# Performance work log

Measured on AMD Instinct MI355X. Metric: run time of the kernel, lower is better.

Reference implementation:

```python
import jax, jax.numpy as jnp
import numpy as np

B, L, H, D = 4096, 256, 32, 2
LOG_PROB_FACTOR = 0.5

def setup_inputs() -> dict:
    key = jax.random.key(0)
    k0, k1, k2, k3 = jax.random.split(key, 4)
    x = jax.random.randint(k0, (B, L), 0, D)  # spin configs in {0,1}
    Wi = jax.random.normal(k1, (D, 4 * H), dtype=jnp.float32) * 0.1   # input kernel (no bias, flax LSTMCell)
    Wh = jax.random.normal(k2, (H, 4 * H), dtype=jnp.float32) * 0.1   # recurrent kernel
    bh = jnp.zeros((4 * H,), dtype=jnp.float32)                        # recurrent bias
    Wo = jax.random.normal(k3, (H, D), dtype=jnp.float32) * 0.1       # output Dense kernel
    bo = jnp.zeros((D,), dtype=jnp.float32)                            # output Dense bias
    return {"x": x, "Wi": Wi, "Wh": Wh, "bh": bh, "Wo": Wo, "bo": bo}

def reference(x, Wi, Wh, bh, Wo, bo):
    # one-hot of spin t-1 (zeros at t=0); log-prob is read out at spin t.
    x_oh = jax.nn.one_hot(x, D, dtype=Wi.dtype)      # [B, L, D]
    xs = jnp.swapaxes(x_oh, 0, 1)                    # [L, B, D] time-major for scan
    c0 = jnp.zeros((x.shape[0], H), Wi.dtype)
    h0 = jnp.zeros((x.shape[0], H), Wi.dtype)
    inp0 = jnp.zeros((x.shape[0], D), Wi.dtype)      # jnp.zeros(inputDim) initial input

    def step(carry, xt):
        c, h, inp = carry
        gates = inp @ Wi + h @ Wh + bh               # [B, 4H]
        i, f, g, o = jnp.split(gates, 4, axis=-1)    # flax LSTMCell gate order i,f,g,o
        c_new = jax.nn.sigmoid(f) * c + jax.nn.sigmoid(i) * jnp.tanh(g)
        h_new = jax.nn.sigmoid(o) * jnp.tanh(c_new)
        out = jax.nn.elu(h_new @ Wo + bo)            # Dense + actFun, [B, D]
        # log(sum(softmax(out) * onehot)) == gathered log_softmax (stable form)
        logp = jnp.sum(jax.nn.log_softmax(out, axis=-1) * xt, axis=-1)  # [B]
        return (c_new, h_new, xt), logp

    _, logps = jax.lax.scan(step, (c0, h0, inp0), xs)  # logps: [L, B]
    return LOG_PROB_FACTOR * jnp.sum(logps, axis=0)    # [B]
```

## Files before the change

### kernel.cpp

```cpp
#include <hip/hip_runtime.h>


typedef __attribute__((ext_vector_type(8))) short bf16x8;
typedef __attribute__((ext_vector_type(4))) float f32x4;

#define LOG2E 1.4426950408889634f
#define LN2   0.6931471805599453f

__device__ __forceinline__ float fexp2(float x) { return __builtin_amdgcn_exp2f(x); }
__device__ __forceinline__ float flog2(float x) { return __builtin_amdgcn_logf(x); }
__device__ __forceinline__ float frcp(float x)  { return __builtin_amdgcn_rcpf(x); }

__device__ __forceinline__ float fsig(float x)   { return frcp(1.f + fexp2(-LOG2E * x)); }
__device__ __forceinline__ float ftanh_(float x) { return 1.f - 2.f * frcp(fexp2(2.f * LOG2E * x) + 1.f); }
__device__ __forceinline__ float felu(float x)   { return x > 0.f ? x : fexp2(LOG2E * x) - 1.f; }

__device__ __forceinline__ unsigned short f2bf(float f) {
    unsigned u = __builtin_bit_cast(unsigned, f);
    u = (u + 0x7FFFu + ((u >> 16) & 1u)) >> 16;
    return (unsigned short)u;
}

constexpr int Bsz = 4096;

__global__ __launch_bounds__(512, 2) void lstm_r10(
    const int*   __restrict__ x,
    const float* __restrict__ Wi,
    const float* __restrict__ Wh,
    const float* __restrict__ bh,
    const float* __restrict__ Wo,
    const float* __restrict__ bo,
    float*       __restrict__ out)
{
    const int tid  = threadIdx.x;
    const int w    = tid >> 6;
    const int lane = tid & 63;
    const int m    = lane & 15;
    const int oct  = lane >> 4;
    const int rot  = w & 3;
    const int half = w >> 2;
    const int b0   = blockIdx.x * 16;

    __shared__ char   spinT[16][260];
    __shared__ float2 Sbuf[256][16];
    __shared__ short  hbuf[2][16][40];
    __shared__ float  red[8][16];

    {
        const int bl = tid >> 5;
        const int c8 = (tid & 31) * 8;
        const int4* src = reinterpret_cast<const int4*>(x + (b0 + bl) * 256 + c8);
        const int4 v0 = src[0], v1 = src[1];
        const int p0 = (v0.x & 1) | ((v0.y & 1) << 8) | ((v0.z & 1) << 16) | ((v0.w & 1) << 24);
        const int p1 = (v1.x & 1) | ((v1.y & 1) << 8) | ((v1.z & 1) << 16) | ((v1.w & 1) << 24);
        *reinterpret_cast<int*>(&spinT[bl][c8])     = p0;
        *reinterpret_cast<int*>(&spinT[bl][c8 + 4]) = p1;
    }

    bf16x8 wfrag[4];
#pragma unroll
    for (int q = 0; q < 4; ++q) {
        const float gs = (q == 2) ? 2.f * LOG2E : -LOG2E;
        const int colg = 32 * q + 16 * half + ((m + rot) & 15);
#pragma unroll
        for (int j = 0; j < 8; ++j)
            wfrag[q][j] = (short)f2bf(gs * Wh[(oct * 8 + j) * 128 + colg]);
    }
    bf16x8 wofragA;
#pragma unroll
    for (int j = 0; j < 8; ++j)
        wofragA[j] = (m < 2) ? (short)f2bf(Wo[(oct * 8 + j) * 2 + m]) : (short)0;

    const int ucell = 4 * oct + rot + 16 * half;
    float bv0[4], bvd[4];
#pragma unroll
    for (int q = 0; q < 4; ++q) {
        const float gs = (q == 2) ? 2.f * LOG2E : -LOG2E;
        const int c0 = 32 * q + ucell;
        bv0[q] = gs * (bh[c0] + Wi[c0]);
        bvd[q] = gs * (Wi[128 + c0] - Wi[c0]);
    }
    const float bo0 = bo[0], bo1 = bo[1];

    float c = fsig(bh[ucell]) * ftanh_(bh[64 + ucell]);
    hbuf[0][m][ucell] = (short)f2bf(fsig(bh[96 + ucell]) * ftanh_(c));
    __syncthreads();

    const f32x4 zero4 = { 0.f, 0.f, 0.f, 0.f };
    f32x4 ccq[4] = { zero4, zero4, zero4, zero4 };

    auto step = [&](const int t, const int rb, const int wb, const float spf) {
        const bf16x8 hfrag =
            *reinterpret_cast<const bf16x8*>(&hbuf[rb][m][8 * oct]);

#pragma unroll
        for (int q = 0; q < 4; ++q) ccq[q][0] = fmaf(spf, bvd[q], bv0[q]);

        f32x4 acc[4];
#pragma unroll
        for (int q = 0; q < 4; ++q)
            acc[q] = __builtin_amdgcn_mfma_f32_16x16x32_bf16(wfrag[q], hfrag, ccq[q], 0, 0, 0);

        if (((t - 1) & 7) == w) {
            const f32x4 hacc =
                __builtin_amdgcn_mfma_f32_16x16x32_bf16(wofragA, hfrag, zero4, 0, 0, 0);
            if (oct == 0) Sbuf[t - 1][m] = make_float2(hacc[0], hacc[1]);
        }

        {
            const float ei = fexp2(acc[0][0]), ef = fexp2(acc[1][0]);
            const float eg = fexp2(acc[2][0]), eo = fexp2(acc[3][0]);
            const float P = (1.f + ei) * (1.f + eg);
            const float Q = 1.f + ef;
            const float R = frcp(P * Q);
            const float gf  = P * R;
            const float igt = (eg - 1.f) * Q * R;
            c = fmaf(gf, c, igt);
            const float ec = fexp2(2.f * LOG2E * c);
            const float h  = (ec - 1.f) * frcp((1.f + eo) * (1.f + ec));
            hbuf[wb][m][ucell] = (short)f2bf(h);
        }
        __syncthreads();
    };

    unsigned sp2 = *reinterpret_cast<const unsigned short*>(&spinT[m][0]);
    for (int tb = 1; tb < 255; tb += 2) {
        const unsigned sp2n =
            *reinterpret_cast<const unsigned short*>(&spinT[m][tb + 1]);
        step(tb,     0, 1, (float)(sp2 & 0xFFu));
        step(tb + 1, 1, 0, (float)(sp2 >> 8));
        sp2 = sp2n;
    }
    step(255, 0, 1, (float)(sp2 & 0xFFu));

    if (w == 7) {
        const bf16x8 hfrag = *reinterpret_cast<const bf16x8*>(&hbuf[1][m][8 * oct]);
        const f32x4 hacc =
            __builtin_amdgcn_mfma_f32_16x16x32_bf16(wofragA, hfrag, zero4, 0, 0, 0);
        if (oct == 0) Sbuf[255][m] = make_float2(hacc[0], hacc[1]);
    }
    __syncthreads();

    float lp = 0.f;
    {
        const int t0 = (w * 4 + oct) * 8;
#pragma unroll
        for (int i = 0; i < 8; ++i) {
            const int t = t0 + i;
            const float2 sv = Sbuf[t][m];
            const int sp = spinT[m][t];
            const float o0 = felu(sv.x + bo0);
            const float o1 = felu(sv.y + bo1);
            const float mx = fmaxf(o0, o1), mn = fminf(o0, o1);
            const float lse = mx + LN2 * flog2(1.f + fexp2(LOG2E * (mn - mx)));
            lp += (sp ? o1 : o0) - lse;
        }
    }
    lp += __shfl_xor(lp, 16, 64);
    lp += __shfl_xor(lp, 32, 64);
    if (lane < 16) red[w][lane] = lp;
    __syncthreads();
    if (tid < 16) {
        float s = 0.f;
#pragma unroll
        for (int ww = 0; ww < 8; ++ww) s += red[ww][tid];
        out[b0 + tid] = 0.5f * s;
    }
}

extern "C" void kernel_launch(void* const* d_in, const int* in_sizes, int n_in,
                              void* d_out, int out_size, void* d_ws, size_t ws_size,
                              hipStream_t stream) {
    const int*   x  = (const int*)d_in[0];
    const float* Wi = (const float*)d_in[1];
    const float* Wh = (const float*)d_in[2];
    const float* bh = (const float*)d_in[3];
    const float* Wo = (const float*)d_in[4];
    const float* bo = (const float*)d_in[5];
    float* out = (float*)d_out;

    lstm_r10<<<dim3(Bsz / 16), dim3(512), 0, stream>>>(x, Wi, Wh, bh, Wo, bo, out);
}
```

Baseline: 136.2 us.

## Shrink LSTM blocks to 4 batch rows with 2 waves and LDS occupancy padding

Each block now handles 4 batch rows with 2 wavefronts instead of 16 rows with 8 wavefronts, giving four times as many blocks. Each wave covers 16 hidden units across all four gates and picks its row's gate value from the MFMA output lanes. The bias is now added after the MFMA instead of being fed in as the accumulator. A dummy 24 KB shared array caps how many blocks fit per CU, so the blocks spread across CUs. The goal is cheaper per-step barriers (2 waves instead of 8) and more independent recurrences per CU, at the cost of 16-wide MFMA tiles that are only a quarter used on the batch dimension.

Result: slower. 157.2 us (+15.4%).

```diff
diff --git a/kernel.cpp b/kernel.cpp
--- a/kernel.cpp
+++ b/kernel.cpp
@@ -23,7 +23,7 @@
 
 constexpr int Bsz = 4096;
 
-__global__ __launch_bounds__(512, 2) void lstm_r10(
+__global__ __launch_bounds__(128, 2) void lstm_r15(
     const int*   __restrict__ x,
     const float* __restrict__ Wi,
     const float* __restrict__ Wh,
@@ -37,14 +37,16 @@
     const int lane = tid & 63;
     const int m    = lane & 15;
     const int oct  = lane >> 4;
-    const int rot  = w & 3;
-    const int half = w >> 2;
-    const int b0   = blockIdx.x * 16;
+    const int b    = m & 3;
+    const int rho  = m >> 2;
+    const int b0   = blockIdx.x * 4;
 
-    __shared__ char   spinT[16][260];
-    __shared__ float2 Sbuf[256][16];
-    __shared__ short  hbuf[2][16][40];
-    __shared__ float  red[8][16];
+    __shared__ char   spinT[4][260];
+    __shared__ float2 Sbuf[256][4];
+    __shared__ __align__(16) short hbuf[2][4][32];
+    __shared__ float  red[2][4];
+    __shared__ char   occ_pad[24576];
+    if ((int)blockIdx.x == -1) occ_pad[0] = (char)tid;
 
     {
         const int bl = tid >> 5;
@@ -61,94 +63,106 @@
 #pragma unroll
     for (int q = 0; q < 4; ++q) {
         const float gs = (q == 2) ? 2.f * LOG2E : -LOG2E;
-        const int colg = 32 * q + 16 * half + ((m + rot) & 15);
+        const int colg = 32 * q + 16 * w + m;
 #pragma unroll
         for (int j = 0; j < 8; ++j)
-            wfrag[q][j] = (short)f2bf(gs * Wh[(oct * 8 + j) * 128 + colg]);
+            wfrag[q][j] = (short)f2bf(gs * Wh[(8 * oct + j) * 128 + colg]);
     }
-    bf16x8 wofragA;
+    bf16x8 wfragO;
 #pragma unroll
     for (int j = 0; j < 8; ++j)
-        wofragA[j] = (m < 2) ? (short)f2bf(Wo[(oct * 8 + j) * 2 + m]) : (short)0;
+        wfragO[j] = (m < 2) ? (short)f2bf(Wo[(8 * oct + j) * 2 + m]) : (short)0;
 
-    const int ucell = 4 * oct + rot + 16 * half;
+    const int u = 16 * w + 4 * oct + rho;
     float bv0[4], bvd[4];
 #pragma unroll
     for (int q = 0; q < 4; ++q) {
         const float gs = (q == 2) ? 2.f * LOG2E : -LOG2E;
-        const int c0 = 32 * q + ucell;
+        const int c0 = 32 * q + u;
         bv0[q] = gs * (bh[c0] + Wi[c0]);
         bvd[q] = gs * (Wi[128 + c0] - Wi[c0]);
     }
     const float bo0 = bo[0], bo1 = bo[1];
 
-    float c = fsig(bh[ucell]) * ftanh_(bh[64 + ucell]);
-    hbuf[0][m][ucell] = (short)f2bf(fsig(bh[96 + ucell]) * ftanh_(c));
+    float c = fsig(bh[u]) * ftanh_(bh[64 + u]);
+    hbuf[0][b][u] = (short)f2bf(fsig(bh[96 + u]) * ftanh_(c));
     __syncthreads();
 
     const f32x4 zero4 = { 0.f, 0.f, 0.f, 0.f };
-    f32x4 ccq[4] = { zero4, zero4, zero4, zero4 };
+    const bool rb0 = (rho & 1) != 0, rb1 = (rho & 2) != 0;
 
-    auto step = [&](const int t, const int rb, const int wb, const float spf) {
+    auto step = [&](const int t, const int rbuf, const int wbuf,
+                    const float spf, const int hw) {
         const bf16x8 hfrag =
-            *reinterpret_cast<const bf16x8*>(&hbuf[rb][m][8 * oct]);
+            *reinterpret_cast<const bf16x8*>(&hbuf[rbuf][b][8 * oct]);
 
-#pragma unroll
-        for (int q = 0; q < 4; ++q) ccq[q][0] = fmaf(spf, bvd[q], bv0[q]);
+        const float cb0 = fmaf(spf, bvd[0], bv0[0]);
+        const float cb1 = fmaf(spf, bvd[1], bv0[1]);
+        const float cb2 = fmaf(spf, bvd[2], bv0[2]);
+        const float cb3 = fmaf(spf, bvd[3], bv0[3]);
 
         f32x4 acc[4];
 #pragma unroll
         for (int q = 0; q < 4; ++q)
-            acc[q] = __builtin_amdgcn_mfma_f32_16x16x32_bf16(wfrag[q], hfrag, ccq[q], 0, 0, 0);
+            acc[q] = __builtin_amdgcn_mfma_f32_16x16x32_bf16(wfrag[q], hfrag, zero4, 0, 0, 0);
 
-        if (((t - 1) & 7) == w) {
-            const f32x4 hacc =
-                __builtin_amdgcn_mfma_f32_16x16x32_bf16(wofragA, hfrag, zero4, 0, 0, 0);
-            if (oct == 0) Sbuf[t - 1][m] = make_float2(hacc[0], hacc[1]);
+        if (w == hw) {
+            const f32x4 aO = __builtin_amdgcn_mfma_f32_16x16x32_bf16(wfragO, hfrag, zero4, 0, 0, 0);
+            if (oct == 0 && m < 4)
+                Sbuf[t - 1][m] = make_float2(aO[0], aO[1]);
         }
 
-        {
-            const float ei = fexp2(acc[0][0]), ef = fexp2(acc[1][0]);
-            const float eg = fexp2(acc[2][0]), eo = fexp2(acc[3][0]);
-            const float P = (1.f + ei) * (1.f + eg);
-            const float Q = 1.f + ef;
-            const float R = frcp(P * Q);
-            const float gf  = P * R;
-            const float igt = (eg - 1.f) * Q * R;
-            c = fmaf(gf, c, igt);
-            const float ec = fexp2(2.f * LOG2E * c);
-            const float h  = (ec - 1.f) * frcp((1.f + eo) * (1.f + ec));
-            hbuf[wb][m][ucell] = (short)f2bf(h);
+        float ge[4];
+#pragma unroll
+        for (int q = 0; q < 4; ++q) {
+            const float s01 = rb0 ? acc[q][1] : acc[q][0];
+            const float s23 = rb0 ? acc[q][3] : acc[q][2];
+            ge[q] = rb1 ? s23 : s01;
         }
+
+        const float a0 = cb0 + ge[0];
+        const float a1 = cb1 + ge[1];
+        const float a2 = cb2 + ge[2];
+        const float a3 = cb3 + ge[3];
+        const float ei = fexp2(a0), ef = fexp2(a1);
+        const float eg = fexp2(a2), eo = fexp2(a3);
+        const float P = (1.f + ei) * (1.f + eg);
+        const float Q = 1.f + ef;
+        const float R = frcp(P * Q);
+        c = fmaf(P * R, c, (eg - 1.f) * Q * R);
+        const float ec = fexp2(2.f * LOG2E * c);
+        const float h  = (ec - 1.f) * frcp((1.f + eo) * (1.f + ec));
+        hbuf[wbuf][b][u] = (short)f2bf(h);
         __syncthreads();
     };
 
-    unsigned sp2 = *reinterpret_cast<const unsigned short*>(&spinT[m][0]);
+    unsigned sp2 = *reinterpret_cast<const unsigned short*>(&spinT[b][0]);
     for (int tb = 1; tb < 255; tb += 2) {
         const unsigned sp2n =
-            *reinterpret_cast<const unsigned short*>(&spinT[m][tb + 1]);
-        step(tb,     0, 1, (float)(sp2 & 0xFFu));
-        step(tb + 1, 1, 0, (float)(sp2 >> 8));
+            *reinterpret_cast<const unsigned short*>(&spinT[b][tb + 1]);
+        step(tb,     0, 1, (float)(sp2 & 0xFFu), 0);
+        step(tb + 1, 1, 0, (float)(sp2 >> 8),    1);
         sp2 = sp2n;
     }
-    step(255, 0, 1, (float)(sp2 & 0xFFu));
+    step(255, 0, 1, (float)(sp2 & 0xFFu), 0);
 
-    if (w == 7) {
-        const bf16x8 hfrag = *reinterpret_cast<const bf16x8*>(&hbuf[1][m][8 * oct]);
-        const f32x4 hacc =
-            __builtin_amdgcn_mfma_f32_16x16x32_bf16(wofragA, hfrag, zero4, 0, 0, 0);
-        if (oct == 0) Sbuf[255][m] = make_float2(hacc[0], hacc[1]);
+    if (w == 1) {
+        const bf16x8 hfrag = *reinterpret_cast<const bf16x8*>(&hbuf[1][b][8 * oct]);
+        const f32x4 aO = __builtin_amdgcn_mfma_f32_16x16x32_bf16(wfragO, hfrag, zero4, 0, 0, 0);
+        if (oct == 0 && m < 4)
+            Sbuf[255][m] = make_float2(aO[0], aO[1]);
     }
     __syncthreads();
 
     float lp = 0.f;
     {
-        const int t0 = (w * 4 + oct) * 8;
+        const int bpost = tid & 3;
+        const int tc    = tid >> 2;
 #pragma unroll
         for (int i = 0; i < 8; ++i) {
-            const int t = t0 + i;
-            const float2 sv = Sbuf[t][m];
-            const int sp = spinT[m][t];
+            const int t = tc * 8 + i;
+            const float2 sv = Sbuf[t][bpost];
+            const int sp = spinT[bpost][t];
             const float o0 = felu(sv.x + bo0);
             const float o1 = felu(sv.y + bo1);
             const float mx = fmaxf(o0, o1), mn = fminf(o0, o1);
@@ -156,16 +170,13 @@
             lp += (sp ? o1 : o0) - lse;
         }
     }
+    lp += __shfl_xor(lp, 4, 64);
+    lp += __shfl_xor(lp, 8, 64);
     lp += __shfl_xor(lp, 16, 64);
     lp += __shfl_xor(lp, 32, 64);
-    if (lane < 16) red[w][lane] = lp;
+    if (lane < 4) red[w][lane] = lp;
     __syncthreads();
-    if (tid < 16) {
-        float s = 0.f;
-#pragma unroll
-        for (int ww = 0; ww < 8; ++ww) s += red[ww][tid];
-        out[b0 + tid] = 0.5f * s;
-    }
+    if (tid < 4) out[b0 + tid] = 0.5f * (red[0][tid] + red[1][tid]);
 }
 
 extern "C" void kernel_launch(void* const* d_in, const int* in_sizes, int n_in,
@@ -179,5 +190,5 @@
     const float* bo = (const float*)d_in[5];
     float* out = (float*)d_out;
 
-    lstm_r10<<<dim3(Bsz / 16), dim3(512), 0, stream>>>(x, Wi, Wh, bh, Wo, bo, out);
+    lstm_r15<<<dim3(Bsz / 4), dim3(128), 0, stream>>>(x, Wi, Wh, bh, Wo, bo, out);
 }
```

## Halve waves per block, give each lane two LSTM cells via gate-interleaved MFMA

Applied to the files above, without the earlier changes.

Reorganizes the recurrent step so a block uses 4 waves instead of 8. Each wave issues two MFMAs whose output columns interleave the i,f,g,o gates, so each lane updates two cells and writes them with one packed bf16 conversion. Fewer waves per block should make each per-step __syncthreads cheaper. A dummy dynamic shared-memory allocation is added to cap blocks per CU, and the epilogue reduction is reworked. The trade-off is more per-lane serial work per step and possibly lower occupancy.

New measurement: 133.7 us. About the same (-1.9%).

```diff
diff --git a/kernel.cpp b/kernel.cpp
--- a/kernel.cpp
+++ b/kernel.cpp
@@ -21,9 +21,15 @@
     return (unsigned short)u;
 }
 
+__device__ __forceinline__ unsigned cvtpk_bf16(float a, float b) {
+    unsigned r;
+    asm("v_cvt_pk_bf16_f32 %0, %1, %2" : "=v"(r) : "v"(a), "v"(b));
+    return r;
+}
+
 constexpr int Bsz = 4096;
 
-__global__ __launch_bounds__(512, 2) void lstm_r10(
+__global__ __launch_bounds__(256, 1) void lstm_r19(
     const int*   __restrict__ x,
     const float* __restrict__ Wi,
     const float* __restrict__ Wh,
@@ -37,133 +43,147 @@
     const int lane = tid & 63;
     const int m    = lane & 15;
     const int oct  = lane >> 4;
-    const int rot  = w & 3;
-    const int half = w >> 2;
     const int b0   = blockIdx.x * 16;
 
+    extern __shared__ char dynpad[];
     __shared__ char   spinT[16][260];
     __shared__ float2 Sbuf[256][16];
     __shared__ short  hbuf[2][16][40];
-    __shared__ float  red[8][16];
-
-    {
-        const int bl = tid >> 5;
-        const int c8 = (tid & 31) * 8;
-        const int4* src = reinterpret_cast<const int4*>(x + (b0 + bl) * 256 + c8);
-        const int4 v0 = src[0], v1 = src[1];
-        const int p0 = (v0.x & 1) | ((v0.y & 1) << 8) | ((v0.z & 1) << 16) | ((v0.w & 1) << 24);
-        const int p1 = (v1.x & 1) | ((v1.y & 1) << 8) | ((v1.z & 1) << 16) | ((v1.w & 1) << 24);
-        *reinterpret_cast<int*>(&spinT[bl][c8])     = p0;
-        *reinterpret_cast<int*>(&spinT[bl][c8 + 4]) = p1;
-    }
-
-    bf16x8 wfrag[4];
-#pragma unroll
-    for (int q = 0; q < 4; ++q) {
-        const float gs = (q == 2) ? 2.f * LOG2E : -LOG2E;
-        const int colg = 32 * q + 16 * half + ((m + rot) & 15);
-#pragma unroll
-        for (int j = 0; j < 8; ++j)
-            wfrag[q][j] = (short)f2bf(gs * Wh[(oct * 8 + j) * 128 + colg]);
-    }
-    bf16x8 wofragA;
+    __shared__ float  red[16][16];
+    if (blockIdx.x == 0xFFFFFFFFu) dynpad[0] = 1;
+
+    {
+        const int bl  = tid >> 4;
+        const int c16 = (tid & 15) * 16;
+        const int4* src = reinterpret_cast<const int4*>(x + (b0 + bl) * 256 + c16);
+#pragma unroll
+        for (int q = 0; q < 4; ++q) {
+            const int4 v = src[q];
+            const int pk = (v.x & 1) | ((v.y & 1) << 8) | ((v.z & 1) << 16) | ((v.w & 1) << 24);
+            *reinterpret_cast<int*>(&spinT[bl][c16 + 4 * q]) = pk;
+        }
+    }
+
+    bf16x8 wfrag[2];
+    {
+        const int r = m & 3;
+        const float gs = (r == 2) ? 2.f * LOG2E : -LOG2E;
+#pragma unroll
+        for (int T = 0; T < 2; ++T) {
+            const int colg = 32 * r + 8 * w + 2 * (m >> 2) + T;
+#pragma unroll
+            for (int j = 0; j < 8; ++j)
+                wfrag[T][j] = (short)f2bf(gs * Wh[(8 * oct + j) * 128 + colg]);
+        }
+    }
+    bf16x8 wfragO;
 #pragma unroll
     for (int j = 0; j < 8; ++j)
-        wofragA[j] = (m < 2) ? (short)f2bf(Wo[(oct * 8 + j) * 2 + m]) : (short)0;
-
-    const int ucell = 4 * oct + rot + 16 * half;
-    float bv0[4], bvd[4];
-#pragma unroll
-    for (int q = 0; q < 4; ++q) {
-        const float gs = (q == 2) ? 2.f * LOG2E : -LOG2E;
-        const int c0 = 32 * q + ucell;
-        bv0[q] = gs * (bh[c0] + Wi[c0]);
-        bvd[q] = gs * (Wi[128 + c0] - Wi[c0]);
+        wfragO[j] = (m < 2) ? (short)f2bf(Wo[(8 * oct + j) * 2 + m]) : (short)0;
+
+    const int uA = 8 * w + 2 * oct;
+    const int uB = uA + 1;
+    float bv0A[4], bvdA[4], bv0B[4], bvdB[4];
+#pragma unroll
+    for (int r = 0; r < 4; ++r) {
+        const float gs = (r == 2) ? 2.f * LOG2E : -LOG2E;
+        const int cA = 32 * r + uA, cB = 32 * r + uB;
+        bv0A[r] = gs * (bh[cA] + Wi[cA]); bvdA[r] = gs * (Wi[128 + cA] - Wi[cA]);
+        bv0B[r] = gs * (bh[cB] + Wi[cB]); bvdB[r] = gs * (Wi[128 + cB] - Wi[cB]);
     }
     const float bo0 = bo[0], bo1 = bo[1];
 
-    float c = fsig(bh[ucell]) * ftanh_(bh[64 + ucell]);
-    hbuf[0][m][ucell] = (short)f2bf(fsig(bh[96 + ucell]) * ftanh_(c));
+    float cA = fsig(bh[uA]) * ftanh_(bh[64 + uA]);
+    float cB = fsig(bh[uB]) * ftanh_(bh[64 + uB]);
+    {
+        const float hA = fsig(bh[96 + uA]) * ftanh_(cA);
+        const float hB = fsig(bh[96 + uB]) * ftanh_(cB);
+        *reinterpret_cast<int*>(&hbuf[0][m][uA]) = (int)cvtpk_bf16(hA, hB);
+    }
     __syncthreads();
 
     const f32x4 zero4 = { 0.f, 0.f, 0.f, 0.f };
-    f32x4 ccq[4] = { zero4, zero4, zero4, zero4 };
-
-    auto step = [&](const int t, const int rb, const int wb, const float spf) {
+
+    auto cellup = [](const f32x4 a, float& cc) -> float {
+        const float ei = fexp2(a[0]), ef = fexp2(a[1]);
+        const float eg = fexp2(a[2]), eo = fexp2(a[3]);
+        const float P = (1.f + ei) * (1.f + eg);
+        const float Q = 1.f + ef;
+        const float R = frcp(P * Q);
+        cc = fmaf(P * R, cc, (eg - 1.f) * Q * R);
+        const float ec = fexp2(2.f * LOG2E * cc);
+        return (ec - 1.f) * frcp((1.f + eo) * (1.f + ec));
+    };
+
+    auto step = [&](const int t, const int rb, const int wb,
+                    const float spf, const int hw) {
         const bf16x8 hfrag =
             *reinterpret_cast<const bf16x8*>(&hbuf[rb][m][8 * oct]);
 
-#pragma unroll
-        for (int q = 0; q < 4; ++q) ccq[q][0] = fmaf(spf, bvd[q], bv0[q]);
-
-        f32x4 acc[4];
-#pragma unroll
-        for (int q = 0; q < 4; ++q)
-            acc[q] = __builtin_amdgcn_mfma_f32_16x16x32_bf16(wfrag[q], hfrag, ccq[q], 0, 0, 0);
-
-        if (((t - 1) & 7) == w) {
-            const f32x4 hacc =
-                __builtin_amdgcn_mfma_f32_16x16x32_bf16(wofragA, hfrag, zero4, 0, 0, 0);
-            if (oct == 0) Sbuf[t - 1][m] = make_float2(hacc[0], hacc[1]);
-        }
-
-        {
-            const float ei = fexp2(acc[0][0]), ef = fexp2(acc[1][0]);
-            const float eg = fexp2(acc[2][0]), eo = fexp2(acc[3][0]);
-            const float P = (1.f + ei) * (1.f + eg);
-            const float Q = 1.f + ef;
-            const float R = frcp(P * Q);
-            const float gf  = P * R;
-            const float igt = (eg - 1.f) * Q * R;
-            c = fmaf(gf, c, igt);
-            const float ec = fexp2(2.f * LOG2E * c);
-            const float h  = (ec - 1.f) * frcp((1.f + eo) * (1.f + ec));
-            hbuf[wb][m][ucell] = (short)f2bf(h);
-        }
+        f32x4 cbA, cbB;
+#pragma unroll
+        for (int r = 0; r < 4; ++r) {
+            cbA[r] = fmaf(spf, bvdA[r], bv0A[r]);
+            cbB[r] = fmaf(spf, bvdB[r], bv0B[r]);
+        }
+
+        const f32x4 accA = __builtin_amdgcn_mfma_f32_16x16x32_bf16(wfrag[0], hfrag, cbA, 0, 0, 0);
+        const f32x4 accB = __builtin_amdgcn_mfma_f32_16x16x32_bf16(wfrag[1], hfrag, cbB, 0, 0, 0);
+
+        if (w == hw) {
+            const f32x4 aO = __builtin_amdgcn_mfma_f32_16x16x32_bf16(wfragO, hfrag, zero4, 0, 0, 0);
+            if (oct == 0) Sbuf[t - 1][m] = make_float2(aO[0], aO[1]);
+        }
+
+        const float hA = cellup(accA, cA);
+        const float hB = cellup(accB, cB);
+        *reinterpret_cast<int*>(&hbuf[wb][m][uA]) = (int)cvtpk_bf16(hA, hB);
         __syncthreads();
     };
 
-    unsigned sp2 = *reinterpret_cast<const unsigned short*>(&spinT[m][0]);
-    for (int tb = 1; tb < 255; tb += 2) {
-        const unsigned sp2n =
-            *reinterpret_cast<const unsigned short*>(&spinT[m][tb + 1]);
-        step(tb,     0, 1, (float)(sp2 & 0xFFu));
-        step(tb + 1, 1, 0, (float)(sp2 >> 8));
-        sp2 = sp2n;
-    }
-    step(255, 0, 1, (float)(sp2 & 0xFFu));
-
-    if (w == 7) {
+    unsigned sp4 = *reinterpret_cast<const unsigned*>(&spinT[m][0]);
+    for (int tb = 1; tb < 253; tb += 4) {
+        const unsigned sp4n =
+            *reinterpret_cast<const unsigned*>(&spinT[m][tb + 3]);
+        step(tb,     0, 1, (float)(sp4 & 0xFFu),         0);
+        step(tb + 1, 1, 0, (float)((sp4 >> 8) & 0xFFu),  1);
+        step(tb + 2, 0, 1, (float)((sp4 >> 16) & 0xFFu), 2);
+        step(tb + 3, 1, 0, (float)(sp4 >> 24),           3);
+        sp4 = sp4n;
+    }
+    step(253, 0, 1, (float)(sp4 & 0xFFu),         0);
+    step(254, 1, 0, (float)((sp4 >> 8) & 0xFFu),  1);
+    step(255, 0, 1, (float)((sp4 >> 16) & 0xFFu), 2);
+
+    if (w == 3) {
         const bf16x8 hfrag = *reinterpret_cast<const bf16x8*>(&hbuf[1][m][8 * oct]);
-        const f32x4 hacc =
-            __builtin_amdgcn_mfma_f32_16x16x32_bf16(wofragA, hfrag, zero4, 0, 0, 0);
-        if (oct == 0) Sbuf[255][m] = make_float2(hacc[0], hacc[1]);
+        const f32x4 aO = __builtin_amdgcn_mfma_f32_16x16x32_bf16(wfragO, hfrag, zero4, 0, 0, 0);
+        if (oct == 0) Sbuf[255][m] = make_float2(aO[0], aO[1]);
     }
     __syncthreads();
 
     float lp = 0.f;
     {
-        const int t0 = (w * 4 + oct) * 8;
-#pragma unroll
-        for (int i = 0; i < 8; ++i) {
-            const int t = t0 + i;
-            const float2 sv = Sbuf[t][m];
-            const int sp = spinT[m][t];
+        const int bpost = tid & 15;
+        const int tc    = tid >> 4;
+#pragma unroll
+        for (int i = 0; i < 16; ++i) {
+            const int t = tc * 16 + i;
+            const float2 sv = Sbuf[t][bpost];
+            const int sp = spinT[bpost][t];
             const float o0 = felu(sv.x + bo0);
             const float o1 = felu(sv.y + bo1);
             const float mx = fmaxf(o0, o1), mn = fminf(o0, o1);
             const float lse = mx + LN2 * flog2(1.f + fexp2(LOG2E * (mn - mx)));
             lp += (sp ? o1 : o0) - lse;
         }
-    }
-    lp += __shfl_xor(lp, 16, 64);
-    lp += __shfl_xor(lp, 32, 64);
-    if (lane < 16) red[w][lane] = lp;
+        red[tc][bpost] = lp;
+    }
     __syncthreads();
     if (tid < 16) {
         float s = 0.f;
 #pragma unroll
-        for (int ww = 0; ww < 8; ++ww) s += red[ww][tid];
+        for (int tc2 = 0; tc2 < 16; ++tc2) s += red[tc2][tid];
         out[b0 + tid] = 0.5f * s;
     }
 }
@@ -179,5 +199,5 @@
     const float* bo = (const float*)d_in[5];
     float* out = (float*)d_out;
 
-    lstm_r10<<<dim3(Bsz / 16), dim3(512), 0, stream>>>(x, Wi, Wh, bh, Wo, bo, out);
-}
+    lstm_r19<<<dim3(Bsz / 16), dim3(256), 45056, stream>>>(x, Wi, Wh, bh, Wo, bo, out);
+}
```
